# Optimization experiments

Measured on AMD Instinct MI355X. Metric: run time of the kernel, lower is better.

The kernel has to match this reference:

```python
import jax, jax.numpy as jnp
import numpy as np
from jax import lax

D_MODEL, D_STATE, D_CONV = 64, 16, 4
D_INNER = 2 * D_MODEL          # expand=2 -> 128
DT_RANK = (D_MODEL + 15) // 16 # 4
DIM_IN, LIN_DIM, DIM_OUT = 5881, 128, 256
B, T = 64, 256


def setup_inputs() -> dict:
    key = jax.random.key(0)
    ks = jax.random.split(key, 20)
    s = 0.02
    inp = {
        "input": jax.random.normal(ks[0], (B, T, DIM_IN), dtype=jnp.float32),
        # encoder (SparseLinear dim_in -> 64)
        "W_enc": jax.random.normal(ks[1], (D_MODEL, DIM_IN), dtype=jnp.float32) * s,
        "b_enc": jax.random.normal(ks[2], (D_MODEL,), dtype=jnp.float32) * s,
        # Mamba params
        "W_in": jax.random.normal(ks[3], (2 * D_INNER, D_MODEL), dtype=jnp.float32) * s,
        "conv_w": jax.random.normal(ks[4], (D_INNER, D_CONV), dtype=jnp.float32) * s,
        "conv_b": jax.random.normal(ks[5], (D_INNER,), dtype=jnp.float32) * s,
        "W_x": jax.random.normal(ks[6], (DT_RANK + 2 * D_STATE, D_INNER), dtype=jnp.float32) * s,
        "W_dt": jax.random.normal(ks[7], (D_INNER, DT_RANK), dtype=jnp.float32) * s,
        "b_dt": jax.random.normal(ks[8], (D_INNER,), dtype=jnp.float32) * s,
        "A_log": jnp.log(jnp.broadcast_to(jnp.arange(1, D_STATE + 1, dtype=jnp.float32), (D_INNER, D_STATE))),
        "D_skip": jnp.ones((D_INNER,), dtype=jnp.float32),
        "W_out": jax.random.normal(ks[9], (D_MODEL, D_INNER), dtype=jnp.float32) * s,
        # heads
        "W_fc": jax.random.normal(ks[10], (LIN_DIM, D_MODEL), dtype=jnp.float32) * s,
        "b_fc": jax.random.normal(ks[11], (LIN_DIM,), dtype=jnp.float32) * s,
        "W_mu": jax.random.normal(ks[12], (DIM_OUT, LIN_DIM), dtype=jnp.float32) * s,
        "b_mu": jax.random.normal(ks[13], (DIM_OUT,), dtype=jnp.float32) * s,
        "W_sig": jax.random.normal(ks[14], (DIM_OUT, LIN_DIM), dtype=jnp.float32) * s,
        "b_sig": jax.random.normal(ks[15], (DIM_OUT,), dtype=jnp.float32) * s,
    }
    return inp


def _mamba(z, W_in, conv_w, conv_b, W_x, W_dt, b_dt, A_log, D_skip, W_out):
    # z: [B, T, d_model]
    xz = jnp.einsum("btm,im->bti", z, W_in)            # [B,T,2*Di]
    x, gate = jnp.split(xz, 2, axis=-1)                 # each [B,T,Di]
    # causal depthwise conv1d, kernel D_CONV
    xp = jnp.pad(x, ((0, 0), (D_CONV - 1, 0), (0, 0)))
    x_conv = sum(xp[:, k:k + x.shape[1], :] * conv_w[:, k] for k in range(D_CONV)) + conv_b
    x_conv = jax.nn.silu(x_conv)
    # input-dependent SSM params
    x_dbl = jnp.einsum("btd,id->bti", x_conv, W_x)      # [B,T,dt_rank+2N]
    dt, Bm, Cm = jnp.split(x_dbl, [DT_RANK, DT_RANK + D_STATE], axis=-1)
    dt = jax.nn.softplus(jnp.einsum("btr,dr->btd", dt, W_dt) + b_dt)  # [B,T,Di]
    A = -jnp.exp(A_log)                                 # [Di,N]
    dA = jnp.exp(dt[..., None] * A)                     # [B,T,Di,N]
    dBx = dt[..., None] * Bm[:, :, None, :] * x_conv[..., None]  # [B,T,Di,N]
    # selective scan over time
    def step(h, inp):
        dA_t, dBx_t, C_t = inp
        h = dA_t * h + dBx_t
        y = jnp.einsum("bdn,bn->bd", h, C_t)
        return h, y
    h0 = jnp.zeros((z.shape[0], D_INNER, D_STATE), dtype=z.dtype)
    _, ys = lax.scan(step, h0, (jnp.moveaxis(dA, 1, 0), jnp.moveaxis(dBx, 1, 0), jnp.moveaxis(Cm, 1, 0)))
    y = jnp.moveaxis(ys, 0, 1) + D_skip * x_conv        # [B,T,Di]
    y = y * jax.nn.silu(gate)
    return jnp.einsum("btd,md->btm", y, W_out)          # [B,T,d_model]


def reference(input, W_enc, b_enc, W_in, conv_w, conv_b, W_x, W_dt, b_dt,
              A_log, D_skip, W_out, W_fc, b_fc, W_mu, b_mu, W_sig, b_sig):
    # per-timestep (sparse) linear encoder, vectorized over time
    z = jnp.einsum("btf,df->btd", input, W_enc) + b_enc   # [B,T,64]
    e = _mamba(z, W_in, conv_w, conv_b, W_x, W_dt, b_dt, A_log, D_skip, W_out)
    e = e.mean(axis=1)                                    # [B,64]; dropout = identity (eval)
    x = jax.nn.elu(jnp.tanh(e @ W_fc.T + b_fc))           # [B,128]
    mu = x @ W_mu.T + b_mu                                # [B,256]
    sigma = jax.nn.elu(x @ W_sig.T + b_sig) + 1.0 + 1e-14 # [B,256]
    return (x, mu, sigma)
```

## Files before the change

### kernel.cpp

```cpp
#include <hip/hip_runtime.h>

typedef unsigned short u16;
typedef unsigned int   u32;

#define BB   64
#define TT   256
#define DIN  5881
#define DM   64
#define DI   128
#define NST  16
#define DTR  4
#define TCH  32
#define NCH  8

#define NROW (BB*TT)
#define NKT  92
#define KQRT 23

#define ZWS_OFF  ((size_t)0)
#define WP_OFF   ((size_t)2*1024*1024)
#define PSG_OFF  ((size_t)3*1024*1024)
#define BC_OFF   ((size_t)35*1024*1024)
#define YS_OFF   ((size_t)37*1024*1024)

__device__ __forceinline__ float bf2f(u16 u) {
    union { u32 i; float f; } v; v.i = ((u32)u) << 16; return v.f;
}
__device__ __forceinline__ u16 f2bf(float f) {
    union { float f; u32 i; } v; v.f = f;
    u32 x = v.i;
    return (u16)((x + 0x7FFFu + ((x >> 16) & 1u)) >> 16);
}

typedef __attribute__((ext_vector_type(8))) short short8;
typedef __attribute__((ext_vector_type(4))) float floatx4;

template<bool BF16>
__device__ __forceinline__ float ld1(const void* p, size_t i) {
    if (BF16) return bf2f(((const u16*)p)[i]);
    else      return ((const float*)p)[i];
}
template<bool BF16>
__device__ __forceinline__ u16 ldb(const void* p, size_t i) {
    if (BF16) return ((const u16*)p)[i];
    else      return f2bf(((const float*)p)[i]);
}
template<bool BF16>
__device__ __forceinline__ void st1(void* p, size_t i, float v) {
    if (BF16) ((u16*)p)[i] = f2bf(v);
    else      ((float*)p)[i] = v;
}

__device__ __forceinline__ short8 as_s8(uint4 v) {
    union { uint4 u; short8 s; } c; c.u = v; return c.s;
}

template<bool BF16>
__device__ __forceinline__ void pack_body(const void* Wenc, u16* wp) {
    int g = blockIdx.x * 256 + threadIdx.x;
    if (g >= NKT * 8 * 64) return;
    int lane = g & 63;  int p = g >> 6;
    int kt = p & 1, nt = (p >> 1) & 3, it = p >> 3;
    int r16 = lane & 15, quad = lane >> 4;
    int n  = nt * 16 + r16;
    int k0 = it * 64 + kt * 32 + quad * 8;
    u32 w[4];
    #pragma unroll
    for (int j = 0; j < 4; ++j) {
        int ka = k0 + 2 * j;
        u32 lo = (ka     < DIN) ? (u32)ldb<BF16>(Wenc, (size_t)n * DIN + ka)     : 0u;
        u32 hi = (ka + 1 < DIN) ? (u32)ldb<BF16>(Wenc, (size_t)n * DIN + ka + 1) : 0u;
        w[j] = lo | (hi << 16);
    }
    *(uint4*)(wp + ((size_t)p * 64 + lane) * 8) = make_uint4(w[0], w[1], w[2], w[3]);
}

__global__ __launch_bounds__(256) void pack_wenc(const void* Wenc, const void* A_log, u16* wp) {
    if (((const u32*)A_log)[0] != 0u) pack_body<true >(Wenc, wp);
    else                              pack_body<false>(Wenc, wp);
}

template<bool BF16>
__device__ __forceinline__ void enc_loadr(const void* inp, int m0, int it, int lane,
                                          u16 (&rg)[16]) {
    const size_t kb = (size_t)it * 64 + lane;
    if (it != NKT - 1) {
        #pragma unroll
        for (int j = 0; j < 16; ++j)
            rg[j] = ldb<BF16>(inp, (size_t)(m0 + j) * DIN + kb);
    } else {
        bool ok = kb < DIN;
        #pragma unroll
        for (int j = 0; j < 16; ++j)
            rg[j] = ok ? ldb<BF16>(inp, (size_t)(m0 + j) * DIN + kb) : (u16)0;
    }
}

__device__ __forceinline__ void enc_loadw(const uint4* wp4, int it, int lane,
                                          uint4 (&b)[8]) {
    const uint4* p = wp4 + (size_t)it * 512 + lane;
    #pragma unroll
    for (int j = 0; j < 8; ++j) b[j] = p[j * 64];
}

__device__ __forceinline__ void enc_write(u16* ms, int lane, const u16 (&rg)[16]) {
    #pragma unroll
    for (int j = 0; j < 16; ++j) ms[j * 72 + lane] = rg[j];
}

__device__ __forceinline__ void enc_compute(const u16* ms, int r16, int quad,
                                            const uint4 (&b)[8], floatx4 (&acc)[4]) {
    short8 a0 = *(const short8*)(ms + r16 * 72 +  0 + quad * 8);
    short8 a1 = *(const short8*)(ms + r16 * 72 + 32 + quad * 8);
    #pragma unroll
    for (int nt = 0; nt < 4; ++nt) {
        acc[nt] = __builtin_amdgcn_mfma_f32_16x16x32_bf16(a0, as_s8(b[nt * 2 + 0]), acc[nt], 0, 0, 0);
        acc[nt] = __builtin_amdgcn_mfma_f32_16x16x32_bf16(a1, as_s8(b[nt * 2 + 1]), acc[nt], 0, 0, 0);
    }
}

template<bool BF16>
__device__ __forceinline__ void enc_body(const void* inp, const void* benc,
                                         const u16* wp, u16* z,
                                         u16* stg, float* zred) {
    const int tid  = threadIdx.x;
    const int wave = tid >> 6, lane = tid & 63;
    const int r16  = lane & 15, quad = lane >> 4;
    const int m0   = blockIdx.x * 16;
    const uint4* wp4 = (const uint4*)wp;
    u16* ms = stg + wave * (16 * 72);
    const int it0 = wave * KQRT;

    floatx4 acc[4];
    #pragma unroll
    for (int nt = 0; nt < 4; ++nt) acc[nt] = (floatx4){0, 0, 0, 0};

    u16   rgA[16], rgB[16];
    uint4 bA[8],  bB[8];
    enc_loadr<BF16>(inp, m0, it0, lane, rgA);
    enc_loadw(wp4, it0, lane, bA);
    int it = it0;
    #pragma unroll 1
    for (int p = 0; p < (KQRT - 1) / 2; ++p, it += 2) {
        enc_write(ms, lane, rgA);
        enc_loadr<BF16>(inp, m0, it + 1, lane, rgB);
        enc_loadw(wp4, it + 1, lane, bB);
        enc_compute(ms, r16, quad, bA, acc);
        enc_write(ms, lane, rgB);
        enc_loadr<BF16>(inp, m0, it + 2, lane, rgA);
        enc_loadw(wp4, it + 2, lane, bA);
        enc_compute(ms, r16, quad, bB, acc);
    }
    enc_write(ms, lane, rgA);
    enc_compute(ms, r16, quad, bA, acc);

    #pragma unroll
    for (int nt = 0; nt < 4; ++nt) {
        int col = nt * 16 + r16;
        #pragma unroll
        for (int reg = 0; reg < 4; ++reg) {
            int row = quad * 4 + reg;
            zred[wave * 1024 + row * 64 + col] = acc[nt][reg];
        }
    }
    __syncthreads();
    #pragma unroll
    for (int rep = 0; rep < 4; ++rep) {
        int o = rep * 256 + tid;
        int col = o & 63;
        float s = zred[o] + zred[1024 + o] + zred[2048 + o] + zred[3072 + o]
                + ld1<BF16>(benc, col);
        z[(size_t)(m0 + (o >> 6)) * DM + col] = f2bf(s);
    }
}

__global__ __launch_bounds__(256, 3) void enc_gemm(const void* inp, const void* benc,
                                                   const void* A_log, const u16* wp, u16* z) {
    __shared__ __align__(16) u16   stg[4 * 16 * 72];
    __shared__ __align__(16) float zred[4 * 1024];
    if (((const u32*)A_log)[0] != 0u) enc_body<true >(inp, benc, wp, z, stg, zred);
    else                              enc_body<false>(inp, benc, wp, z, stg, zred);
}

template<bool BF16>
__device__ __forceinline__ void prep_body(
        const void* W_in, const void* conv_w, const void* conv_b,
        const void* W_x, const void* W_dt, const void* b_dt, const void* D_skip,
        const u16* zws, float4* psg, float* BCg,
        u16* zc, u16* xl, u16* gl, u16* xcb, float* xd2) {

    const int bid  = blockIdx.x;
    const int b    = bid >> 3, c = bid & 7;
    const int tid  = threadIdx.x;
    const int wave = tid >> 6, lane = tid & 63;
    const int quad = lane >> 4, r16 = lane & 15;
    const int dd   = tid & 127;

    float cw[4], cb, wdt[4], bdt, Dv;
    #pragma unroll
    for (int k = 0; k < 4; ++k) cw[k] = ld1<BF16>(conv_w, dd * 4 + k);
    cb = ld1<BF16>(conv_b, dd);
    #pragma unroll
    for (int r = 0; r < 4; ++r) wdt[r] = ld1<BF16>(W_dt, dd * 4 + r);
    bdt = ld1<BF16>(b_dt, dd);
    Dv  = ld1<BF16>(D_skip, dd);

    short8 win[4][2];
    #pragma unroll
    for (int nt = 0; nt < 4; ++nt)
        #pragma unroll
        for (int kt = 0; kt < 2; ++kt) {
            size_t base = (size_t)(wave * 64 + nt * 16 + r16) * DM + kt * 32 + quad * 8;
            short8 v;
            #pragma unroll
            for (int e = 0; e < 8; ++e) v[e] = (short)ldb<BF16>(W_in, base + e);
            win[nt][kt] = v;
        }

    short8 wx[4];
    {
        int j = wave * 16 + r16;
        #pragma unroll
        for (int kt = 0; kt < 4; ++kt) {
            short8 v = (short8){0,0,0,0,0,0,0,0};
            if (wave < 3 && j < DTR + 2 * NST) {
                size_t base = (size_t)j * DI + kt * 32 + quad * 8;
                #pragma unroll
                for (int e = 0; e < 8; ++e) v[e] = (short)ldb<BF16>(W_x, base + e);
            }
            wx[kt] = v;
        }
    }

    const int base_t = c * 32 - 16;
    for (int i = tid; i < 48 * 64; i += 256) {
        int rr = i >> 6, nn = i & 63, t = base_t + rr;
        u16 v = 0;
        if (t >= 0) v = zws[(size_t)(b * TT + t) * DM + nn];
        zc[rr * 72 + nn] = v;
    }
    __syncthreads();

    floatx4 xza[3][4];
    #pragma unroll
    for (int mt = 0; mt < 3; ++mt)
        #pragma unroll
        for (int nt = 0; nt < 4; ++nt) xza[mt][nt] = (floatx4){0,0,0,0};
    #pragma unroll
    for (int kt = 0; kt < 2; ++kt) {
        short8 a[3];
        #pragma unroll
        for (int mt = 0; mt < 3; ++mt)
            a[mt] = *(const short8*)(&zc[(mt * 16 + r16) * 72 + kt * 32 + quad * 8]);
        #pragma unroll
        for (int nt = 0; nt < 4; ++nt)
            #pragma unroll
            for (int mt = 0; mt < 3; ++mt)
                xza[mt][nt] = __builtin_amdgcn_mfma_f32_16x16x32_bf16(a[mt], win[nt][kt], xza[mt][nt], 0, 0, 0);
    }
    #pragma unroll
    for (int mt = 0; mt < 3; ++mt)
        #pragma unroll
        for (int nt = 0; nt < 4; ++nt) {
            int n = wave * 64 + nt * 16 + r16;
            #pragma unroll
            for (int reg = 0; reg < 4; ++reg) {
                int rr = mt * 16 + quad * 4 + reg;
                u16 v = f2bf(xza[mt][nt][reg]);
                if (n < DI) { if (rr >= 13) xl[(rr - 13) * 128 + n] = v; }
                else if (rr >= 16) gl[(rr - 16) * 128 + (n - DI)] = v;
            }
        }
    __syncthreads();

    for (int it2 = tid; it2 < TCH * DI; it2 += 256) {
        int t = it2 >> 7, d = it2 & 127;
        float a = cb;
        #pragma unroll
        for (int k = 0; k < 4; ++k) a += bf2f(xl[(t + k) * 128 + d]) * cw[k];
        float s = a / (1.f + expf(-a));
        xcb[t * 136 + d] = f2bf(s);
    }
    __syncthreads();

    {
        floatx4 xda0 = (floatx4){0,0,0,0}, xda1 = (floatx4){0,0,0,0};
        if (wave < 3) {
            #pragma unroll
            for (int kt = 0; kt < 4; ++kt) {
                short8 a0 = *(const short8*)(&xcb[(0 * 16 + r16) * 136 + kt * 32 + quad * 8]);
                short8 a1 = *(const short8*)(&xcb[(1 * 16 + r16) * 136 + kt * 32 + quad * 8]);
                xda0 = __builtin_amdgcn_mfma_f32_16x16x32_bf16(a0, wx[kt], xda0, 0, 0, 0);
                xda1 = __builtin_amdgcn_mfma_f32_16x16x32_bf16(a1, wx[kt], xda1, 0, 0, 0);
            }
            int j = wave * 16 + r16;
            if (j < DTR + 2 * NST) {
                #pragma unroll
                for (int reg = 0; reg < 4; ++reg) {
                    xd2[(0 * 16 + quad * 4 + reg) * 40 + j] = xda0[reg];
                    xd2[(1 * 16 + quad * 4 + reg) * 40 + j] = xda1[reg];
                }
            }
        }
    }
    __syncthreads();

    const size_t rowb = (size_t)b * TT + c * 32;
    for (int it2 = tid; it2 < TCH * DI; it2 += 256) {
        int t = it2 >> 7, d = it2 & 127;
        float v = bdt;
        #pragma unroll
        for (int r = 0; r < 4; ++r) v += xd2[t * 40 + r] * wdt[r];
        float sp  = (v > 20.f) ? v : log1pf(expf(v));
        float xcv = bf2f(xcb[t * 136 + d]);
        float g   = bf2f(gl[t * 128 + d]);
        float sg  = g / (1.f + expf(-g));
        psg[(rowb + t) * DI + d] = make_float4(sp, sp * xcv, sg, Dv * xcv * sg);
    }
    for (int i = tid; i < TCH * 32; i += 256) {
        int t = i >> 5, j = i & 31;
        BCg[(rowb + t) * 32 + j] = xd2[t * 40 + DTR + j];
    }
}

__global__ __launch_bounds__(256) void prep(
        const void* W_in, const void* conv_w, const void* conv_b,
        const void* W_x, const void* W_dt, const void* b_dt, const void* D_skip,
        const void* A_log, const u16* zws, float4* psg, float* BCg) {
    __shared__ __align__(16) u16  zc[48 * 72];
    __shared__ __align__(16) u16  xl[35 * 128];
    __shared__ __align__(16) u16  gl[32 * 128];
    __shared__ __align__(16) u16  xcb[32 * 136];
    __shared__ __align__(16) float xd2[32 * 40];
    if (((const u32*)A_log)[0] != 0u)
        prep_body<true >(W_in, conv_w, conv_b, W_x, W_dt, b_dt, D_skip, zws, psg, BCg,
                         zc, xl, gl, xcb, xd2);
    else
        prep_body<false>(W_in, conv_w, conv_b, W_x, W_dt, b_dt, D_skip, zws, psg, BCg,
                         zc, xl, gl, xcb, xd2);
}

__device__ __forceinline__ void scan_ld(const float4* psg, const float* BCg,
        size_t pbase, size_t bbase, int s, float4 (&P)[8], float (&Bv)[8], float (&Cv)[8]) {
    #pragma unroll
    for (int q = 0; q < 8; ++q) {
        int r = s * 8 + q;
        P[q]  = psg[pbase + (size_t)r * DI];
        Bv[q] = BCg[bbase + (size_t)r * 32];
        Cv[q] = BCg[bbase + (size_t)r * 32 + 16];
    }
}
__device__ __forceinline__ void scan_cmp(const float4 (&P)[8], const float (&Bv)[8],
        const float (&Cv)[8], float Av, int n, float& h, float& acc, float& sk) {
    #pragma unroll
    for (int q = 0; q < 8; ++q) {
        float e = expf(P[q].x * Av);
        h   = fmaf(e, h, P[q].y * Bv[q]);
        acc = fmaf(h * Cv[q], P[q].z, acc);
        sk += (n == 0) ? P[q].w : 0.f;
    }
}

__global__ __launch_bounds__(512) void scan_k(const void* A_log, const float4* psg,
        const float* BCg, float* ysg) {
    const int tid = threadIdx.x;
    const int b = blockIdx.x >> 2, dq = blockIdx.x & 3;
    const int dl = tid >> 4, n = tid & 15;
    const int d = dq * 32 + dl;
    const bool isbf = (((const u32*)A_log)[0] != 0u);
    float al = isbf ? bf2f(((const u16*)A_log)[d * NST + n])
                    : ((const float*)A_log)[d * NST + n];
    const float Av = -expf(al);
    const size_t rb = (size_t)b * TT;
    const size_t pbase = rb * DI + d;
    const size_t bbase = rb * 32 + n;

    float4 pA[8], pB[8];
    float  BA[8], CA[8], Bb[8], Cb[8];
    float h = 0.f, acc = 0.f, sk = 0.f;

    scan_ld(psg, BCg, pbase, bbase, 0, pA, BA, CA);
    for (int s = 0; s < 32; s += 2) {
        scan_ld(psg, BCg, pbase, bbase, s + 1, pB, Bb, Cb);
        scan_cmp(pA, BA, CA, Av, n, h, acc, sk);
        if (s + 2 < 32) scan_ld(psg, BCg, pbase, bbase, s + 2, pA, BA, CA);
        scan_cmp(pB, Bb, Cb, Av, n, h, acc, sk);
    }
    acc += __shfl_xor(acc, 1);
    acc += __shfl_xor(acc, 2);
    acc += __shfl_xor(acc, 4);
    acc += __shfl_xor(acc, 8);
    if (n == 0) ysg[(size_t)b * DI + d] = acc + sk;
}

template<bool BF16>
__device__ __forceinline__ void heads_body(
        const void* W_out, const void* W_fc, const void* b_fc,
        const void* W_mu, const void* b_mu, const void* W_sig, const void* b_sig,
        const float* ysg, void* out, float* yb, float* es, float* xs) {
    const int b = blockIdx.x, tid = threadIdx.x;
    if (tid < DI) yb[tid] = ysg[(size_t)b * DI + tid] * (1.f / (float)TT);
    __syncthreads();
    if (tid < DM) {
        float s = 0.f;
        #pragma unroll 8
        for (int k = 0; k < DI; ++k) s += yb[k] * ld1<BF16>(W_out, (size_t)tid * DI + k);
        es[tid] = s;
    }
    __syncthreads();
    if (tid < 128) {
        float s = ld1<BF16>(b_fc, tid);
        #pragma unroll 8
        for (int k = 0; k < DM; ++k) s += es[k] * ld1<BF16>(W_fc, (size_t)tid * DM + k);
        float th = tanhf(s);
        float xv = th > 0.f ? th : expm1f(th);
        xs[tid] = xv;
        st1<BF16>(out, (size_t)b * 128 + tid, xv);
    }
    __syncthreads();
    for (int j = tid; j < 512; j += 256) {
        int o = j & 255;
        bool is_mu = (j < 256);
        const void* w = is_mu ? W_mu : W_sig;
        float s = ld1<BF16>(is_mu ? b_mu : b_sig, o);
        #pragma unroll 8
        for (int k = 0; k < 128; ++k) s += xs[k] * ld1<BF16>(w, (size_t)o * 128 + k);
        if (is_mu) {
            st1<BF16>(out, 8192 + (size_t)b * 256 + o, s);
        } else {
            float e = s > 0.f ? s : expm1f(s);
            st1<BF16>(out, 8192 + 16384 + (size_t)b * 256 + o, e + 1.f + 1e-14f);
        }
    }
}

__global__ __launch_bounds__(256) void heads_k(
        const void* W_out, const void* W_fc, const void* b_fc,
        const void* W_mu, const void* b_mu, const void* W_sig, const void* b_sig,
        const void* A_log, const float* ysg, void* out) {
    __shared__ float yb[128];
    __shared__ float es[64];
    __shared__ float xs[128];
    if (((const u32*)A_log)[0] != 0u)
        heads_body<true >(W_out, W_fc, b_fc, W_mu, b_mu, W_sig, b_sig, ysg, out, yb, es, xs);
    else
        heads_body<false>(W_out, W_fc, b_fc, W_mu, b_mu, W_sig, b_sig, ysg, out, yb, es, xs);
}

extern "C" void kernel_launch(void* const* d_in, const int* in_sizes, int n_in,
                              void* d_out, int out_size, void* d_ws, size_t ws_size,
                              hipStream_t stream) {
    (void)in_sizes; (void)n_in; (void)ws_size; (void)out_size;
    char* ws = (char*)d_ws;
    u16*    zws = (u16*)(ws + ZWS_OFF);
    u16*    wp  = (u16*)(ws + WP_OFF);
    float4* psg = (float4*)(ws + PSG_OFF);
    float*  BCg = (float*)(ws + BC_OFF);
    float*  ysg = (float*)(ws + YS_OFF);

    pack_wenc<<<184, 256, 0, stream>>>(d_in[1], d_in[9], wp);
    enc_gemm<<<1024, 256, 0, stream>>>(d_in[0], d_in[2], d_in[9], wp, zws);
    prep<<<512, 256, 0, stream>>>(d_in[3], d_in[4], d_in[5], d_in[6], d_in[7],
                                  d_in[8], d_in[10], d_in[9], zws, psg, BCg);
    scan_k<<<256, 512, 0, stream>>>(d_in[9], psg, BCg, ysg);
    heads_k<<<64, 256, 0, stream>>>(d_in[11], d_in[12], d_in[13], d_in[14],
                                    d_in[15], d_in[16], d_in[17], d_in[9], ysg, d_out);
}
```

Before: 635.3 us.

## Double encoder GEMM row tile to 32 rows to reuse packed weight fragments

The encoder GEMM block now handles 32 rows instead of 16. Each wave runs two M sub-tiles against the same loaded W_enc fragments, which halves weight traffic per output row and halves the grid to 512 blocks. The software pipeline drops from double-buffered registers to a single buffer, and the occupancy hint in launch bounds is removed. This raises register and LDS use per block, may lower occupancy, and exposes more load latency because the input is huge and bandwidth-bound.

```diff
diff --git a/kernel.cpp b/kernel.cpp
--- a/kernel.cpp
+++ b/kernel.cpp
@@ -16,6 +16,7 @@
 #define NROW (BB*TT)
 #define NKT  92
 #define KQRT 23
+#define MRT  32
 
 #define ZWS_OFF  ((size_t)0)
 #define WP_OFF   ((size_t)2*1024*1024)
@@ -81,17 +82,17 @@
 }
 
 template<bool BF16>
-__device__ __forceinline__ void enc_loadr(const void* inp, int m0, int it, int lane,
-                                          u16 (&rg)[16]) {
+__device__ __forceinline__ void enc_loadr32(const void* inp, int m0, int it, int lane,
+                                            u16 (&rg)[MRT]) {
     const size_t kb = (size_t)it * 64 + lane;
     if (it != NKT - 1) {
         #pragma unroll
-        for (int j = 0; j < 16; ++j)
+        for (int j = 0; j < MRT; ++j)
             rg[j] = ldb<BF16>(inp, (size_t)(m0 + j) * DIN + kb);
     } else {
         bool ok = kb < DIN;
         #pragma unroll
-        for (int j = 0; j < 16; ++j)
+        for (int j = 0; j < MRT; ++j)
             rg[j] = ok ? ldb<BF16>(inp, (size_t)(m0 + j) * DIN + kb) : (u16)0;
     }
 }
@@ -103,19 +104,22 @@
     for (int j = 0; j < 8; ++j) b[j] = p[j * 64];
 }
 
-__device__ __forceinline__ void enc_write(u16* ms, int lane, const u16 (&rg)[16]) {
-    #pragma unroll
-    for (int j = 0; j < 16; ++j) ms[j * 72 + lane] = rg[j];
-}
-
-__device__ __forceinline__ void enc_compute(const u16* ms, int r16, int quad,
-                                            const uint4 (&b)[8], floatx4 (&acc)[4]) {
-    short8 a0 = *(const short8*)(ms + r16 * 72 +  0 + quad * 8);
-    short8 a1 = *(const short8*)(ms + r16 * 72 + 32 + quad * 8);
-    #pragma unroll
-    for (int nt = 0; nt < 4; ++nt) {
-        acc[nt] = __builtin_amdgcn_mfma_f32_16x16x32_bf16(a0, as_s8(b[nt * 2 + 0]), acc[nt], 0, 0, 0);
-        acc[nt] = __builtin_amdgcn_mfma_f32_16x16x32_bf16(a1, as_s8(b[nt * 2 + 1]), acc[nt], 0, 0, 0);
+__device__ __forceinline__ void enc_write32(u16* ms, int lane, const u16 (&rg)[MRT]) {
+    #pragma unroll
+    for (int j = 0; j < MRT; ++j) ms[j * 72 + lane] = rg[j];
+}
+
+__device__ __forceinline__ void enc_compute2(const u16* ms, int r16, int quad,
+                                             const uint4 (&b)[8], floatx4 (&acc)[2][4]) {
+    #pragma unroll
+    for (int mt = 0; mt < 2; ++mt) {
+        short8 a0 = *(const short8*)(ms + (mt * 16 + r16) * 72 +  0 + quad * 8);
+        short8 a1 = *(const short8*)(ms + (mt * 16 + r16) * 72 + 32 + quad * 8);
+        #pragma unroll
+        for (int nt = 0; nt < 4; ++nt) {
+            acc[mt][nt] = __builtin_amdgcn_mfma_f32_16x16x32_bf16(a0, as_s8(b[nt * 2 + 0]), acc[mt][nt], 0, 0, 0);
+            acc[mt][nt] = __builtin_amdgcn_mfma_f32_16x16x32_bf16(a1, as_s8(b[nt * 2 + 1]), acc[mt][nt], 0, 0, 0);
+        }
     }
 }
 
@@ -126,58 +130,58 @@
     const int tid  = threadIdx.x;
     const int wave = tid >> 6, lane = tid & 63;
     const int r16  = lane & 15, quad = lane >> 4;
-    const int m0   = blockIdx.x * 16;
+    const int m0   = blockIdx.x * MRT;
     const uint4* wp4 = (const uint4*)wp;
-    u16* ms = stg + wave * (16 * 72);
+    u16* ms = stg + wave * (MRT * 72);
     const int it0 = wave * KQRT;
 
-    floatx4 acc[4];
-    #pragma unroll
-    for (int nt = 0; nt < 4; ++nt) acc[nt] = (floatx4){0, 0, 0, 0};
-
-    u16   rgA[16], rgB[16];
-    uint4 bA[8],  bB[8];
-    enc_loadr<BF16>(inp, m0, it0, lane, rgA);
+    floatx4 acc[2][4];
+    #pragma unroll
+    for (int mt = 0; mt < 2; ++mt)
+        #pragma unroll
+        for (int nt = 0; nt < 4; ++nt) acc[mt][nt] = (floatx4){0, 0, 0, 0};
+
+    u16   rgA[MRT];
+    uint4 bA[8];
+    enc_loadr32<BF16>(inp, m0, it0, lane, rgA);
     enc_loadw(wp4, it0, lane, bA);
-    int it = it0;
     #pragma unroll 1
-    for (int p = 0; p < (KQRT - 1) / 2; ++p, it += 2) {
-        enc_write(ms, lane, rgA);
-        enc_loadr<BF16>(inp, m0, it + 1, lane, rgB);
-        enc_loadw(wp4, it + 1, lane, bB);
-        enc_compute(ms, r16, quad, bA, acc);
-        enc_write(ms, lane, rgB);
-        enc_loadr<BF16>(inp, m0, it + 2, lane, rgA);
-        enc_loadw(wp4, it + 2, lane, bA);
-        enc_compute(ms, r16, quad, bB, acc);
-    }
-    enc_write(ms, lane, rgA);
-    enc_compute(ms, r16, quad, bA, acc);
-
-    #pragma unroll
-    for (int nt = 0; nt < 4; ++nt) {
-        int col = nt * 16 + r16;
-        #pragma unroll
-        for (int reg = 0; reg < 4; ++reg) {
-            int row = quad * 4 + reg;
-            zred[wave * 1024 + row * 64 + col] = acc[nt][reg];
-        }
-    }
-    __syncthreads();
-    #pragma unroll
-    for (int rep = 0; rep < 4; ++rep) {
+    for (int p = 0; p < KQRT; ++p) {
+        const int it = it0 + p;
+        enc_write32(ms, lane, rgA);
+        if (p + 1 < KQRT)
+            enc_loadr32<BF16>(inp, m0, it + 1, lane, rgA);
+        enc_compute2(ms, r16, quad, bA, acc);
+        if (p + 1 < KQRT)
+            enc_loadw(wp4, it + 1, lane, bA);
+    }
+
+    #pragma unroll
+    for (int mt = 0; mt < 2; ++mt)
+        #pragma unroll
+        for (int nt = 0; nt < 4; ++nt) {
+            int col = nt * 16 + r16;
+            #pragma unroll
+            for (int reg = 0; reg < 4; ++reg) {
+                int row = mt * 16 + quad * 4 + reg;
+                zred[wave * (MRT * 64) + row * 64 + col] = acc[mt][nt][reg];
+            }
+        }
+    __syncthreads();
+    #pragma unroll
+    for (int rep = 0; rep < (MRT * 64) / 256; ++rep) {
         int o = rep * 256 + tid;
         int col = o & 63;
-        float s = zred[o] + zred[1024 + o] + zred[2048 + o] + zred[3072 + o]
+        float s = zred[o] + zred[2048 + o] + zred[4096 + o] + zred[6144 + o]
                 + ld1<BF16>(benc, col);
         z[(size_t)(m0 + (o >> 6)) * DM + col] = f2bf(s);
     }
 }
 
-__global__ __launch_bounds__(256, 3) void enc_gemm(const void* inp, const void* benc,
-                                                   const void* A_log, const u16* wp, u16* z) {
-    __shared__ __align__(16) u16   stg[4 * 16 * 72];
-    __shared__ __align__(16) float zred[4 * 1024];
+__global__ __launch_bounds__(256) void enc_gemm(const void* inp, const void* benc,
+                                                const void* A_log, const u16* wp, u16* z) {
+    __shared__ __align__(16) u16   stg[4 * MRT * 72];
+    __shared__ __align__(16) float zred[4 * MRT * 64];
     if (((const u32*)A_log)[0] != 0u) enc_body<true >(inp, benc, wp, z, stg, zred);
     else                              enc_body<false>(inp, benc, wp, z, stg, zred);
 }
@@ -459,7 +463,7 @@
     float*  ysg = (float*)(ws + YS_OFF);
 
     pack_wenc<<<184, 256, 0, stream>>>(d_in[1], d_in[9], wp);
-    enc_gemm<<<1024, 256, 0, stream>>>(d_in[0], d_in[2], d_in[9], wp, zws);
+    enc_gemm<<<512, 256, 0, stream>>>(d_in[0], d_in[2], d_in[9], wp, zws);
     prep<<<512, 256, 0, stream>>>(d_in[3], d_in[4], d_in[5], d_in[6], d_in[7],
                                   d_in[8], d_in[10], d_in[9], zws, psg, BCg);
     scan_k<<<256, 512, 0, stream>>>(d_in[9], psg, BCg, ysg);
```

Measured after the change: 631.9 us. No clear change (-0.5%).
